# Optimization experiments

Hardware: AMD Instinct MI355X
Metric: run time of the kernel (lower is better)

## Reference

```python
import jax, jax.numpy as jnp
import numpy as np
from jax import lax

H, D_INNER, G, D_GATE, K, DH = 2560, 8192, 32, 4096, 4, 128
EPS = 1e-6


def setup_inputs() -> dict:
    key = jax.random.key(0)
    ks = jax.random.split(key, 9)
    B, L = 2, 4096
    s = 0.02
    return {
        "hidden_states": jax.random.normal(ks[0], (B, L, H), jnp.float32),
        "W_qkv": jax.random.normal(ks[1], (D_INNER, H), jnp.float32) * s,
        "W_b": jax.random.normal(ks[2], (G, H), jnp.float32) * s,
        "W_a": jax.random.normal(ks[3], (G, H), jnp.float32) * s,
        "conv_w": jax.random.normal(ks[4], (D_INNER, 1, K), jnp.float32) * s,
        "W_out": jax.random.normal(ks[5], (H, D_GATE), jnp.float32) * s,
        "norm_w": jnp.ones((DH,), jnp.float32),
        "A_log": jax.random.normal(ks[6], (G,), jnp.float32) * 0.1,
        "dt_bias": jax.random.normal(ks[7], (G,), jnp.float32) * 0.1,
    }


def _ssm_scan(x, B_coeff, C_coeff, A_log, dt_bias):
    # x: [B,L,G,DH], B_coeff/C_coeff: [B,L,G]
    A = -jnp.exp(A_log.astype(jnp.float32))          # [G]
    dt = jax.nn.softplus(dt_bias.astype(jnp.float32))  # [G]
    dA = jnp.exp(dt * A)                              # [G], time-invariant decay
    xf = x.astype(jnp.float32).transpose(1, 0, 2, 3)      # [L,B,G,DH]
    Bf = B_coeff.astype(jnp.float32).transpose(1, 0, 2)   # [L,B,G]
    Cf = C_coeff.astype(jnp.float32).transpose(1, 0, 2)
    h0 = jnp.zeros(x.shape[0:1] + (G, DH), jnp.float32)   # [B,G,DH]

    def step(h, inp):
        x_t, b_t, c_t = inp
        h = dA[None, :, None] * h + (dt * b_t)[..., None] * x_t
        return h, c_t[..., None] * h

    _, ys = lax.scan(step, h0, (xf, Bf, Cf))  # ys: [L,B,G,DH]
    return ys.transpose(1, 0, 2, 3).astype(x.dtype)


def reference(hidden_states, W_qkv, W_b, W_a, conv_w, W_out, norm_w, A_log, dt_bias):
    Bsz, L, _ = hidden_states.shape
    xz = hidden_states @ W_qkv.T           # [B,L,8192]
    B_coeff = hidden_states @ W_b.T        # [B,L,32]
    C_coeff = hidden_states @ W_a.T        # [B,L,32]
    # causal depthwise conv1d (padding K-1 on left, right pad trimmed)
    xz_c = lax.conv_general_dilated(
        xz.transpose(0, 2, 1), conv_w, (1,), [(K - 1, 0)],
        feature_group_count=D_INNER,
        dimension_numbers=("NCH", "OIH", "NCH"))
    xz_c = xz_c.transpose(0, 2, 1)          # [B,L,8192]
    x, z_inner = jnp.split(xz_c, 2, axis=-1)  # each [B,L,4096]
    x = jax.nn.silu(x).reshape(Bsz, L, G, DH)
    y = _ssm_scan(x, B_coeff, C_coeff, A_log, dt_bias)  # [B,L,G,DH]
    # RMSNorm over head_dim
    y = y * lax.rsqrt(jnp.mean(y * y, axis=-1, keepdims=True) + EPS) * norm_w
    y = y.reshape(Bsz, L, D_GATE) * jax.nn.silu(z_inner)
    return y @ W_out.T                      # [B,L,2560]
```

## Files before the change

### kernel.cpp

```cpp
#include <hip/hip_runtime.h>
#include <cstdint>
#include <cstddef>

#define H_DIM   2560
#define DINNER  8192
#define GHEADS  32
#define DGATE   4096
#define DH      128
#define BSZ     2
#define LSEQ    4096
#define MROWS   (BSZ*LSEQ)
#define NXPAD   4352
#define NCHUNK  64
#define SCHUNK  (LSEQ/NCHUNK)

typedef __attribute__((ext_vector_type(4))) float    f32x4;
typedef __attribute__((ext_vector_type(8))) _Float16 f16x8;
typedef unsigned short u16;
typedef unsigned int   u32;

static __device__ __forceinline__ u16 f2h(float f) {
  _Float16 h = (_Float16)f;
  union { _Float16 h; u16 u; } v; v.h = h; return v.u;
}
static __device__ __forceinline__ float h2f(u16 u) {
  union { u16 u; _Float16 h; } v; v.u = u; return (float)v.h;
}
static __device__ __forceinline__ float silu(float x) {
  return x / (1.0f + expf(-x));
}

__global__ void cast_f32_f16(const float* __restrict__ in, u16* __restrict__ out, int n4) {
  int i = blockIdx.x * blockDim.x + threadIdx.x;
  if (i < n4) {
    f32x4 v = ((const f32x4*)in)[i];
    u32 p0 = (u32)f2h(v[0]) | ((u32)f2h(v[1]) << 16);
    u32 p1 = (u32)f2h(v[2]) | ((u32)f2h(v[3]) << 16);
    ((uint2*)out)[i] = make_uint2(p0, p1);
  }
}

__global__ void build_wc(const float* __restrict__ Wqkv, const float* __restrict__ Wb,
                         const float* __restrict__ Wa, u16* __restrict__ wcp,
                         u16* __restrict__ wz) {
  int row = blockIdx.x;
  if (row >= NXPAD) {
    const float* src = Wqkv + (size_t)(4096 + row - NXPAD) * H_DIM;
    u16* oh = wz + (size_t)(row - NXPAD) * H_DIM;
    for (int i = threadIdx.x; i < H_DIM / 4; i += blockDim.x) {
      f32x4 v = ((const f32x4*)src)[i];
      ((uint2*)oh)[i] = make_uint2((u32)f2h(v[0]) | ((u32)f2h(v[1]) << 16),
                                   (u32)f2h(v[2]) | ((u32)f2h(v[3]) << 16));
    }
    return;
  }
  const float* src = nullptr;
  if (row < 4096)              src = Wqkv + (size_t)row * H_DIM;
  else if (row < 4128)         src = Wb + (size_t)(row - 4096) * H_DIM;
  else if (row < 4160)         src = Wa + (size_t)(row - 4128) * H_DIM;
  u16* oh = wcp + (size_t)row * H_DIM;
  for (int i = threadIdx.x; i < H_DIM / 4; i += blockDim.x) {
    u32 p0 = 0, p1 = 0;
    if (src) {
      f32x4 v = ((const f32x4*)src)[i];
      p0 = (u32)f2h(v[0]) | ((u32)f2h(v[1]) << 16);
      p1 = (u32)f2h(v[2]) | ((u32)f2h(v[3]) << 16);
    }
    ((uint2*)oh)[i] = make_uint2(p0, p1);
  }
}

static __device__ __forceinline__ void gload16(const u16* g, u16* l) {
  __builtin_amdgcn_global_load_lds(
      (const __attribute__((address_space(1))) u32*)g,
      (__attribute__((address_space(3))) u32*)l, 16, 0, 0);
}

template<bool OUT_F16>
__global__ __launch_bounds__(512)
void gemm_h(const u16* __restrict__ A, const u16* __restrict__ Bt,
            void* __restrict__ Cout, int K, int ldc, int nbx, int cpx) {
  __shared__ __align__(16) u16 As0[128 * 32];
  __shared__ __align__(16) u16 As1[128 * 32];
  __shared__ __align__(16) u16 Bs0[256 * 32];
  __shared__ __align__(16) u16 Bs1[256 * 32];
  const int tid  = threadIdx.x;
  const int lane = tid & 63;
  const int wave = tid >> 6;
  const int wm = (wave & 1) * 64;
  const int wn = (wave >> 1) * 64;
  const int bid = blockIdx.x;
  const int lsw = (bid & 7) * cpx + (bid >> 3);
  const int by  = lsw / nbx;
  const int bx  = lsw - by * nbx;
  const size_t bm = (size_t)by * 128;
  const size_t bn = (size_t)bx * 256;

  const int eA = tid * 8;
  const int rA = eA >> 5, cA = eA & 31;
  const int rB0 = rA, cB0 = cA;
  const int rB1 = 128 + rA;

  const u16* Ab = A + bm * (size_t)K;
  const u16* Bb = Bt + bn * (size_t)K;

  f32x4 acc[4][4];
#pragma unroll
  for (int i = 0; i < 4; i++)
#pragma unroll
    for (int j = 0; j < 4; j++) acc[i][j] = (f32x4){0.f, 0.f, 0.f, 0.f};

#define STAGE(AS, BS, kk)                                              \
  do {                                                                 \
    gload16(Ab + (size_t)rA * K + (kk) + cA, &AS[wave * 512]);         \
    gload16(Bb + (size_t)rB0 * K + (kk) + cB0, &BS[wave * 512]);       \
    gload16(Bb + (size_t)rB1 * K + (kk) + cB0, &BS[4096 + wave * 512]);\
  } while (0)

#define COMPUTE(AS, BS)                                                          \
  do {                                                                           \
    const int fr = lane & 15, fk = (lane >> 4) * 8;                              \
    f16x8 av[4], bv[4];                                                          \
    _Pragma("unroll")                                                            \
    for (int i = 0; i < 4; i++) av[i] = *(const f16x8*)&AS[(wm + i * 16 + fr) * 32 + fk]; \
    _Pragma("unroll")                                                            \
    for (int j = 0; j < 4; j++) bv[j] = *(const f16x8*)&BS[(wn + j * 16 + fr) * 32 + fk]; \
    _Pragma("unroll")                                                            \
    for (int i = 0; i < 4; i++)                                                  \
      _Pragma("unroll")                                                          \
      for (int j = 0; j < 4; j++)                                                \
        acc[i][j] = __builtin_amdgcn_mfma_f32_16x16x32_f16(av[i], bv[j], acc[i][j], 0, 0, 0); \
  } while (0)

  STAGE(As0, Bs0, 0);
  __syncthreads();
  for (int k0 = 0; k0 < K; k0 += 64) {
    if (k0 + 32 < K) STAGE(As1, Bs1, k0 + 32);
    COMPUTE(As0, Bs0);
    __syncthreads();
    if (k0 + 64 < K) STAGE(As0, Bs0, k0 + 64);
    COMPUTE(As1, Bs1);
    __syncthreads();
  }
#undef STAGE
#undef COMPUTE

  const int cr = (lane >> 4) * 4, ccol = lane & 15;
#pragma unroll
  for (int i = 0; i < 4; i++)
#pragma unroll
    for (int j = 0; j < 4; j++)
#pragma unroll
      for (int r = 0; r < 4; r++) {
        size_t row = bm + wm + i * 16 + cr + r;
        size_t col = bn + wn + j * 16 + ccol;
        if (OUT_F16) ((u16*)Cout)[row * ldc + col] = f2h(acc[i][j][r]);
        else         ((float*)Cout)[row * ldc + col] = acc[i][j][r];
      }
}

__global__ __launch_bounds__(64)
void scan_pass1(const float* __restrict__ xzx, const float* __restrict__ conv_w,
                const float* __restrict__ A_log, const float* __restrict__ dt_bias,
                float* __restrict__ E) {
  const int bid = blockIdx.x;
  const int c   = bid & (NCHUNK - 1);
  const int bg  = bid >> 6;
  const int g   = bg & (GHEADS - 1);
  const int b   = bg >> 5;
  const int lane = threadIdx.x;
  const int ch0 = g * DH + lane, ch1 = ch0 + 64;

  const f32x4 w0 = ((const f32x4*)conv_w)[ch0];
  const f32x4 w1 = ((const f32x4*)conv_w)[ch1];
  const float dt = log1pf(expf(dt_bias[g]));
  const float Ac = -expf(A_log[g]);
  const float dA = expf(dt * Ac);

  const int l0 = c * SCHUNK;
  const float* base = xzx + (size_t)b * LSEQ * NXPAD;

  float xm3 = 0, xm2 = 0, xm1 = 0, Xm3 = 0, Xm2 = 0, Xm1 = 0;
#pragma unroll
  for (int j = 0; j < 3; j++) {
    int l = l0 - 3 + j;
    float v0 = 0, v1 = 0;
    if (l >= 0) {
      const float* rp = base + (size_t)l * NXPAD;
      v0 = rp[ch0]; v1 = rp[ch1];
    }
    if (j == 0) { xm3 = v0; Xm3 = v1; }
    else if (j == 1) { xm2 = v0; Xm2 = v1; }
    else { xm1 = v0; Xm1 = v1; }
  }
  float h0 = 0.f, h1 = 0.f;
  for (int t = 0; t < SCHUNK; t++) {
    const float* rp = base + (size_t)(l0 + t) * NXPAD;
    float xc0 = rp[ch0], xc1 = rp[ch1];
    float cx0 = w0[0] * xm3 + w0[1] * xm2 + w0[2] * xm1 + w0[3] * xc0;
    float cx1 = w1[0] * Xm3 + w1[1] * Xm2 + w1[2] * Xm1 + w1[3] * xc1;
    xm3 = xm2; xm2 = xm1; xm1 = xc0;
    Xm3 = Xm2; Xm2 = Xm1; Xm1 = xc1;
    float u = dt * rp[DGATE + g];
    h0 = dA * h0 + u * silu(cx0);
    h1 = dA * h1 + u * silu(cx1);
  }
  float* ep = E + (size_t)bid * DH;
  ep[lane] = h0; ep[lane + 64] = h1;
}

__global__ __launch_bounds__(64)
void scan_pass2(const float* __restrict__ E, float* __restrict__ Hs,
                const float* __restrict__ A_log, const float* __restrict__ dt_bias) {
  const int bg = blockIdx.x;
  const int g = bg & (GHEADS - 1);
  const int lane = threadIdx.x;
  const float dt = log1pf(expf(dt_bias[g]));
  const float Ac = -expf(A_log[g]);
  const float dAS = expf(dt * Ac * (float)SCHUNK);
  float h0 = 0.f, h1 = 0.f;
  for (int c = 0; c < NCHUNK; c++) {
    size_t idx = ((size_t)bg * NCHUNK + c) * DH;
    Hs[idx + lane] = h0; Hs[idx + lane + 64] = h1;
    h0 = dAS * h0 + E[idx + lane];
    h1 = dAS * h1 + E[idx + lane + 64];
  }
}

__global__ __launch_bounds__(64)
void scan_pass3(const float* __restrict__ xzx, const u16* __restrict__ xzz,
                const float* __restrict__ conv_w,
                const float* __restrict__ A_log, const float* __restrict__ dt_bias,
                const float* __restrict__ norm_w, const float* __restrict__ Hs,
                u16* __restrict__ gbuf) {
  const int bid = blockIdx.x;
  const int c   = bid & (NCHUNK - 1);
  const int bg  = bid >> 6;
  const int g   = bg & (GHEADS - 1);
  const int b   = bg >> 5;
  const int lane = threadIdx.x;
  const int ch0 = g * DH + lane, ch1 = ch0 + 64;

  const f32x4 wx0 = ((const f32x4*)conv_w)[ch0];
  const f32x4 wx1 = ((const f32x4*)conv_w)[ch1];
  const f32x4 wz0 = ((const f32x4*)conv_w)[DGATE + ch0];
  const f32x4 wz1 = ((const f32x4*)conv_w)[DGATE + ch1];
  const float nw0 = norm_w[lane], nw1 = norm_w[lane + 64];

  const float dt = log1pf(expf(dt_bias[g]));
  const float Ac = -expf(A_log[g]);
  const float dA = expf(dt * Ac);

  const int l0 = c * SCHUNK;
  const float* basex = xzx + (size_t)b * LSEQ * NXPAD;
  const u16*   basez = xzz + (size_t)b * LSEQ * DGATE;

  float xm3 = 0, xm2 = 0, xm1 = 0, Xm3 = 0, Xm2 = 0, Xm1 = 0;
  float zm3 = 0, zm2 = 0, zm1 = 0, Zm3 = 0, Zm2 = 0, Zm1 = 0;
#pragma unroll
  for (int j = 0; j < 3; j++) {
    int l = l0 - 3 + j;
    float vx0 = 0, vx1 = 0, vz0 = 0, vz1 = 0;
    if (l >= 0) {
      const float* rp = basex + (size_t)l * NXPAD;
      const u16*   rz = basez + (size_t)l * DGATE;
      vx0 = rp[ch0]; vx1 = rp[ch1];
      vz0 = h2f(rz[ch0]); vz1 = h2f(rz[ch1]);
    }
    if (j == 0) { xm3 = vx0; Xm3 = vx1; zm3 = vz0; Zm3 = vz1; }
    else if (j == 1) { xm2 = vx0; Xm2 = vx1; zm2 = vz0; Zm2 = vz1; }
    else { xm1 = vx0; Xm1 = vx1; zm1 = vz0; Zm1 = vz1; }
  }
  float h0 = Hs[(size_t)bid * DH + lane];
  float h1 = Hs[(size_t)bid * DH + lane + 64];
  for (int t = 0; t < SCHUNK; t++) {
    const int l = l0 + t;
    const float* rp = basex + (size_t)l * NXPAD;
    const u16*   rz = basez + (size_t)l * DGATE;
    float xc0 = rp[ch0], xc1 = rp[ch1];
    float zc0 = h2f(rz[ch0]), zc1 = h2f(rz[ch1]);
    float cx0 = wx0[0] * xm3 + wx0[1] * xm2 + wx0[2] * xm1 + wx0[3] * xc0;
    float cx1 = wx1[0] * Xm3 + wx1[1] * Xm2 + wx1[2] * Xm1 + wx1[3] * xc1;
    float cz0 = wz0[0] * zm3 + wz0[1] * zm2 + wz0[2] * zm1 + wz0[3] * zc0;
    float cz1 = wz1[0] * Zm3 + wz1[1] * Zm2 + wz1[2] * Zm1 + wz1[3] * zc1;
    xm3 = xm2; xm2 = xm1; xm1 = xc0;  Xm3 = Xm2; Xm2 = Xm1; Xm1 = xc1;
    zm3 = zm2; zm2 = zm1; zm1 = zc0;  Zm3 = Zm2; Zm2 = Zm1; Zm1 = zc1;
    float bcl = rp[DGATE + g];
    float ccl = rp[DGATE + 32 + g];
    float u = dt * bcl;
    h0 = dA * h0 + u * silu(cx0);
    h1 = dA * h1 + u * silu(cx1);
    float y0 = ccl * h0, y1 = ccl * h1;
    float ss = y0 * y0 + y1 * y1;
    ss += __shfl_xor(ss, 32); ss += __shfl_xor(ss, 16); ss += __shfl_xor(ss, 8);
    ss += __shfl_xor(ss, 4);  ss += __shfl_xor(ss, 2);  ss += __shfl_xor(ss, 1);
    const float sc = rsqrtf(ss * (1.0f / DH) + 1e-6f);
    u16* op = gbuf + (size_t)(b * LSEQ + l) * DGATE + g * DH;
    op[lane]      = f2h(y0 * sc * nw0 * silu(cz0));
    op[lane + 64] = f2h(y1 * sc * nw1 * silu(cz1));
  }
}

extern "C" void kernel_launch(void* const* d_in, const int* in_sizes, int n_in,
                              void* d_out, int out_size, void* d_ws, size_t ws_size,
                              hipStream_t stream) {
  (void)in_sizes; (void)n_in; (void)out_size; (void)ws_size;
  const float* hs    = (const float*)d_in[0];
  const float* Wqkv  = (const float*)d_in[1];
  const float* Wb    = (const float*)d_in[2];
  const float* Wa    = (const float*)d_in[3];
  const float* convw = (const float*)d_in[4];
  const float* Wout  = (const float*)d_in[5];
  const float* normw = (const float*)d_in[6];
  const float* Alog  = (const float*)d_in[7];
  const float* dtb   = (const float*)d_in[8];
  float* out = (float*)d_out;

  char* ws = (char*)d_ws;
  size_t off = 0;
  auto alloc = [&](size_t bytes) { void* p = ws + off; off += (bytes + 255) & ~(size_t)255; return p; };
  float* xzx    = (float*)alloc((size_t)MROWS * NXPAD * 4);
  u16*   xzz    = (u16*)alloc((size_t)MROWS * DGATE * 2);
  u16*   wcp    = (u16*)alloc((size_t)NXPAD * H_DIM * 2);
  u16*   wz     = (u16*)alloc((size_t)DGATE * H_DIM * 2);
  (void)alloc((size_t)24 << 20);
  u16*   wout_h = (u16*)alloc((size_t)H_DIM * DGATE * 2);
  float* E      = (float*)alloc((size_t)BSZ * GHEADS * NCHUNK * DH * 4);
  float* Hst    = (float*)alloc((size_t)BSZ * GHEADS * NCHUNK * DH * 4);
  u16*   gbuf   = wcp;
  u16*   hs_h   = (u16*)d_out;

  const int n4_hs = MROWS * H_DIM / 4;
  cast_f32_f16<<<(n4_hs + 255) / 256, 256, 0, stream>>>(hs, hs_h, n4_hs);
  build_wc<<<NXPAD + DGATE, 256, 0, stream>>>(Wqkv, Wb, Wa, wcp, wz);
  const int n4_wo = H_DIM * DGATE / 4;
  cast_f32_f16<<<(n4_wo + 255) / 256, 256, 0, stream>>>(Wout, wout_h, n4_wo);

  gemm_h<false><<<1088, 512, 0, stream>>>(hs_h, wcp, xzx, H_DIM, NXPAD, 17, 136);
  gemm_h<true><<<1024, 512, 0, stream>>>(hs_h, wz, xzz, H_DIM, DGATE, 16, 128);

  scan_pass1<<<BSZ * GHEADS * NCHUNK, 64, 0, stream>>>(xzx, convw, Alog, dtb, E);
  scan_pass2<<<BSZ * GHEADS, 64, 0, stream>>>(E, Hst, Alog, dtb);
  scan_pass3<<<BSZ * GHEADS * NCHUNK, 64, 0, stream>>>(xzx, xzz, convw, Alog, dtb, normw, Hst, gbuf);

  gemm_h<false><<<640, 512, 0, stream>>>(gbuf, wout_h, out, DGATE, H_DIM, 10, 80);
}
```

Before: 860.4 us.

## Swizzle GEMM LDS layout and deepen async prefetch with partial vmcnt waits

Stores each 32-element k-slice in LDS with an XOR swizzle on the 8-element column groups, so the fragment reads avoid bank conflicts. Both LDS buffers are now prefetched ahead, and explicit s_waitcnt vmcnt(3) plus raw s_barrier replace __syncthreads, letting one stage's global-to-LDS loads stay in flight while the other buffer is consumed. It also raises wave priority around the MFMA block. The manual waitcnt/barrier scheme relies on exact counts of outstanding loads and adds extra barriers per iteration.

New measurement: 854.5 us. Within noise of the previous version (-0.7%).

```diff
diff --git a/kernel.cpp b/kernel.cpp
--- a/kernel.cpp
+++ b/kernel.cpp
@@ -75,6 +75,10 @@
       (const __attribute__((address_space(1))) u32*)g,
       (__attribute__((address_space(3))) u32*)l, 16, 0, 0);
 }
+
+#define BAR()    asm volatile("s_barrier" ::: "memory")
+#define WAITV3() asm volatile("s_waitcnt vmcnt(3)" ::: "memory")
+#define WAITV0() asm volatile("s_waitcnt vmcnt(0)" ::: "memory")
 
 template<bool OUT_F16>
 __global__ __launch_bounds__(512)
@@ -96,11 +100,8 @@
   const size_t bm = (size_t)by * 128;
   const size_t bn = (size_t)bx * 256;
 
-  const int eA = tid * 8;
-  const int rA = eA >> 5, cA = eA & 31;
-  const int rB0 = rA, cB0 = cA;
-  const int rB1 = 128 + rA;
-
+  const int srow = tid >> 2;
+  const int scol = (((tid & 3) ^ ((srow >> 1) & 3)) << 3);
   const u16* Ab = A + bm * (size_t)K;
   const u16* Bb = Bt + bn * (size_t)K;
 
@@ -110,37 +111,46 @@
 #pragma unroll
     for (int j = 0; j < 4; j++) acc[i][j] = (f32x4){0.f, 0.f, 0.f, 0.f};
 
-#define STAGE(AS, BS, kk)                                              \
-  do {                                                                 \
-    gload16(Ab + (size_t)rA * K + (kk) + cA, &AS[wave * 512]);         \
-    gload16(Bb + (size_t)rB0 * K + (kk) + cB0, &BS[wave * 512]);       \
-    gload16(Bb + (size_t)rB1 * K + (kk) + cB0, &BS[4096 + wave * 512]);\
+#define STAGE(AS, BS, kk)                                                \
+  do {                                                                   \
+    gload16(Ab + (size_t)srow * K + (kk) + scol, &AS[tid * 8]);          \
+    gload16(Bb + (size_t)srow * K + (kk) + scol, &BS[tid * 8]);          \
+    gload16(Bb + (size_t)(128 + srow) * K + (kk) + scol, &BS[4096 + tid * 8]); \
   } while (0)
 
-#define COMPUTE(AS, BS)                                                          \
-  do {                                                                           \
-    const int fr = lane & 15, fk = (lane >> 4) * 8;                              \
-    f16x8 av[4], bv[4];                                                          \
-    _Pragma("unroll")                                                            \
-    for (int i = 0; i < 4; i++) av[i] = *(const f16x8*)&AS[(wm + i * 16 + fr) * 32 + fk]; \
-    _Pragma("unroll")                                                            \
-    for (int j = 0; j < 4; j++) bv[j] = *(const f16x8*)&BS[(wn + j * 16 + fr) * 32 + fk]; \
-    _Pragma("unroll")                                                            \
-    for (int i = 0; i < 4; i++)                                                  \
-      _Pragma("unroll")                                                          \
-      for (int j = 0; j < 4; j++)                                                \
+#define COMPUTE(AS, BS)                                                           \
+  do {                                                                            \
+    const int fr = lane & 15;                                                     \
+    const int fo = (((lane >> 4) ^ ((fr >> 1) & 3)) << 3);    \
+    f16x8 av[4], bv[4];                                                           \
+    _Pragma("unroll")                                                             \
+    for (int i = 0; i < 4; i++) av[i] = *(const f16x8*)&AS[(wm + i * 16 + fr) * 32 + fo]; \
+    _Pragma("unroll")                                                             \
+    for (int j = 0; j < 4; j++) bv[j] = *(const f16x8*)&BS[(wn + j * 16 + fr) * 32 + fo]; \
+    __builtin_amdgcn_s_setprio(1);                                                \
+    _Pragma("unroll")                                                             \
+    for (int i = 0; i < 4; i++)                                                   \
+      _Pragma("unroll")                                                           \
+      for (int j = 0; j < 4; j++)                                                 \
         acc[i][j] = __builtin_amdgcn_mfma_f32_16x16x32_f16(av[i], bv[j], acc[i][j], 0, 0, 0); \
+    __builtin_amdgcn_s_setprio(0);                                                \
   } while (0)
 
   STAGE(As0, Bs0, 0);
-  __syncthreads();
+  STAGE(As1, Bs1, 32);
+  WAITV3();
+  BAR();
   for (int k0 = 0; k0 < K; k0 += 64) {
-    if (k0 + 32 < K) STAGE(As1, Bs1, k0 + 32);
     COMPUTE(As0, Bs0);
-    __syncthreads();
-    if (k0 + 64 < K) STAGE(As0, Bs0, k0 + 64);
+    BAR();
+    if (k0 + 64 < K) { STAGE(As0, Bs0, k0 + 64); WAITV3(); }
+    else             { WAITV0(); }
+    BAR();
     COMPUTE(As1, Bs1);
-    __syncthreads();
+    BAR();
+    if (k0 + 96 < K) { STAGE(As1, Bs1, k0 + 96); WAITV3(); }
+    else             { WAITV0(); }
+    BAR();
   }
 #undef STAGE
 #undef COMPUTE
```

## Replace GEMM with 256x256-tile kernel using swizzled LDS and interleaved pipeline

Applied to the files above, without the earlier changes.

The fp16 MFMA GEMM moves from 128x256 tiles with a 32-wide K step to 256x256 tiles with a 64-wide K step, so each wave holds 8x4 accumulator fragments. LDS rows are XOR-swizzled to avoid bank conflicts. The main loop interleaves async global-to-LDS loads, LDS reads and MFMA groups, using explicit s_barrier, vmcnt waits and s_setprio. The intent is more reuse per loaded byte and better overlap of memory and compute in all three GEMMs. The cost is fewer blocks (320–544), about 128KB of LDS per block, and higher register pressure.

New measurement: 854.1 us. About the same (-0.7%).

```diff
diff --git a/kernel.cpp b/kernel.cpp
--- a/kernel.cpp
+++ b/kernel.cpp
@@ -76,86 +76,127 @@
       (__attribute__((address_space(3))) u32*)l, 16, 0, 0);
 }
 
+#define BAR()    asm volatile("s_barrier" ::: "memory")
+#define WAITV4() asm volatile("s_waitcnt vmcnt(4)" ::: "memory")
+#define WAITV0() asm volatile("s_waitcnt vmcnt(0)" ::: "memory")
+
 template<bool OUT_F16>
-__global__ __launch_bounds__(512)
-void gemm_h(const u16* __restrict__ A, const u16* __restrict__ Bt,
-            void* __restrict__ Cout, int K, int ldc, int nbx, int cpx) {
-  __shared__ __align__(16) u16 As0[128 * 32];
-  __shared__ __align__(16) u16 As1[128 * 32];
-  __shared__ __align__(16) u16 Bs0[256 * 32];
-  __shared__ __align__(16) u16 Bs1[256 * 32];
+__global__ __launch_bounds__(512, 2)
+void gemm256(const u16* __restrict__ A, const u16* __restrict__ Bt,
+             void* __restrict__ Cout, int K, int ldc, int nbx, int cpx) {
+  __shared__ __align__(16) u16 As[2][256 * 64];
+  __shared__ __align__(16) u16 Bs[2][256 * 64];
   const int tid  = threadIdx.x;
   const int lane = tid & 63;
   const int wave = tid >> 6;
-  const int wm = (wave & 1) * 64;
-  const int wn = (wave >> 1) * 64;
-  const int bid = blockIdx.x;
-  const int lsw = (bid & 7) * cpx + (bid >> 3);
-  const int by  = lsw / nbx;
-  const int bx  = lsw - by * nbx;
-  const size_t bm = (size_t)by * 128;
-  const size_t bn = (size_t)bx * 256;
-
-  const int eA = tid * 8;
-  const int rA = eA >> 5, cA = eA & 31;
-  const int rB0 = rA, cB0 = cA;
-  const int rB1 = 128 + rA;
-
-  const u16* Ab = A + bm * (size_t)K;
-  const u16* Bb = Bt + bn * (size_t)K;
-
-  f32x4 acc[4][4];
-#pragma unroll
-  for (int i = 0; i < 4; i++)
+  const int wm   = wave & 1;
+  const int wn   = wave >> 1;
+  const int bid  = blockIdx.x;
+  const int lsw  = (bid & 7) * cpx + (bid >> 3);
+  const int by   = lsw / nbx;
+  const int bx   = lsw - by * nbx;
+  const u16* Ab = A  + (size_t)by * 256 * K;
+  const u16* Bb = Bt + (size_t)bx * 256 * K;
+
+  const int srow0 = tid >> 3;
+  const int scol  = (((tid & 7) ^ (srow0 & 7)) << 3);
+  const int fr  = lane & 15;
+  const int kg  = lane >> 4;
+  const int rsw = fr & 7;
+
+  f32x4 acc[8][4];
+#pragma unroll
+  for (int i = 0; i < 8; i++)
 #pragma unroll
     for (int j = 0; j < 4; j++) acc[i][j] = (f32x4){0.f, 0.f, 0.f, 0.f};
 
-#define STAGE(AS, BS, kk)                                              \
-  do {                                                                 \
-    gload16(Ab + (size_t)rA * K + (kk) + cA, &AS[wave * 512]);         \
-    gload16(Bb + (size_t)rB0 * K + (kk) + cB0, &BS[wave * 512]);       \
-    gload16(Bb + (size_t)rB1 * K + (kk) + cB0, &BS[4096 + wave * 512]);\
+  f16x8 av[4], bv[4];
+
+#define STAGEOP(dst, gb, kk)                                                     \
+  do {                                                                           \
+    _Pragma("unroll")                                                            \
+    for (int q = 0; q < 4; q++)                                                  \
+      gload16((gb) + (size_t)(srow0 + q * 64) * K + (kk) + scol,                 \
+              (dst) + (size_t)(q * 512 + tid) * 8);                              \
   } while (0)
 
-#define COMPUTE(AS, BS)                                                          \
+#define DSREAD_AV(d, qm, s)                                                      \
   do {                                                                           \
-    const int fr = lane & 15, fk = (lane >> 4) * 8;                              \
-    f16x8 av[4], bv[4];                                                          \
     _Pragma("unroll")                                                            \
-    for (int i = 0; i < 4; i++) av[i] = *(const f16x8*)&AS[(wm + i * 16 + fr) * 32 + fk]; \
+    for (int i = 0; i < 4; i++)                                                  \
+      av[i] = *(const f16x8*)&As[d][(wm * 128 + (qm) * 64 + i * 16 + fr) * 64 +  \
+                                    ((((s) * 4 + kg) ^ rsw) << 3)];              \
+  } while (0)
+
+#define DSREAD_BV(d, s)                                                          \
+  do {                                                                           \
     _Pragma("unroll")                                                            \
-    for (int j = 0; j < 4; j++) bv[j] = *(const f16x8*)&BS[(wn + j * 16 + fr) * 32 + fk]; \
+    for (int j = 0; j < 4; j++)                                                  \
+      bv[j] = *(const f16x8*)&Bs[d][(wn * 64 + j * 16 + fr) * 64 +               \
+                                    ((((s) * 4 + kg) ^ rsw) << 3)];              \
+  } while (0)
+
+#define MFMA16(qm)                                                               \
+  do {                                                                           \
+    __builtin_amdgcn_s_setprio(1);                                               \
     _Pragma("unroll")                                                            \
     for (int i = 0; i < 4; i++)                                                  \
       _Pragma("unroll")                                                          \
       for (int j = 0; j < 4; j++)                                                \
-        acc[i][j] = __builtin_amdgcn_mfma_f32_16x16x32_f16(av[i], bv[j], acc[i][j], 0, 0, 0); \
+        acc[(qm) * 4 + i][j] =                                                   \
+            __builtin_amdgcn_mfma_f32_16x16x32_f16(av[i], bv[j],                 \
+                                                   acc[(qm) * 4 + i][j], 0, 0, 0);\
+    __builtin_amdgcn_s_setprio(0);                                               \
   } while (0)
 
-  STAGE(As0, Bs0, 0);
-  __syncthreads();
-  for (int k0 = 0; k0 < K; k0 += 64) {
-    if (k0 + 32 < K) STAGE(As1, Bs1, k0 + 32);
-    COMPUTE(As0, Bs0);
-    __syncthreads();
-    if (k0 + 64 < K) STAGE(As0, Bs0, k0 + 64);
-    COMPUTE(As1, Bs1);
-    __syncthreads();
-  }
-#undef STAGE
-#undef COMPUTE
+  const int T = K >> 7;
+  STAGEOP(&Bs[0][0], Bb, 0);
+  STAGEOP(&As[0][0], Ab, 0);
+  STAGEOP(&Bs[1][0], Bb, 64);
+  WAITV4();
+  BAR();
+
+  for (int it = 0; it < T; ++it) {
+    const int k0 = it << 7;
+    const bool lastit = (it == T - 1);
+    DSREAD_BV(0, 0); DSREAD_AV(0, 0, 0);
+    STAGEOP(&As[1][0], Ab, k0 + 64);
+    BAR(); MFMA16(0); BAR();
+    DSREAD_AV(0, 1, 0);
+    BAR(); MFMA16(1); BAR();
+    DSREAD_BV(0, 1); DSREAD_AV(0, 0, 1);
+    BAR(); MFMA16(0); BAR();
+    DSREAD_AV(0, 1, 1);
+    if (!lastit) { STAGEOP(&Bs[0][0], Bb, k0 + 128); WAITV4(); }
+    else         { WAITV0(); }
+    BAR(); MFMA16(1); BAR();
+    DSREAD_BV(1, 0); DSREAD_AV(1, 0, 0);
+    if (!lastit) STAGEOP(&As[0][0], Ab, k0 + 128);
+    BAR(); MFMA16(0); BAR();
+    DSREAD_AV(1, 1, 0);
+    BAR(); MFMA16(1); BAR();
+    DSREAD_BV(1, 1); DSREAD_AV(1, 0, 1);
+    BAR(); MFMA16(0); BAR();
+    DSREAD_AV(1, 1, 1);
+    if (!lastit) { STAGEOP(&Bs[1][0], Bb, k0 + 192); WAITV4(); }
+    BAR(); MFMA16(1); BAR();
+  }
+#undef STAGEOP
+#undef DSREAD_AV
+#undef DSREAD_BV
+#undef MFMA16
 
   const int cr = (lane >> 4) * 4, ccol = lane & 15;
 #pragma unroll
-  for (int i = 0; i < 4; i++)
-#pragma unroll
-    for (int j = 0; j < 4; j++)
+  for (int mf = 0; mf < 8; mf++)
+#pragma unroll
+    for (int nf = 0; nf < 4; nf++)
 #pragma unroll
       for (int r = 0; r < 4; r++) {
-        size_t row = bm + wm + i * 16 + cr + r;
-        size_t col = bn + wn + j * 16 + ccol;
-        if (OUT_F16) ((u16*)Cout)[row * ldc + col] = f2h(acc[i][j][r]);
-        else         ((float*)Cout)[row * ldc + col] = acc[i][j][r];
+        size_t row = (size_t)by * 256 + wm * 128 + mf * 16 + cr + r;
+        size_t col = (size_t)bx * 256 + wn * 64 + nf * 16 + ccol;
+        if (OUT_F16) ((u16*)Cout)[row * ldc + col] = f2h(acc[mf][nf][r]);
+        else         ((float*)Cout)[row * ldc + col] = acc[mf][nf][r];
       }
 }
 
@@ -336,12 +377,12 @@
   const int n4_wo = H_DIM * DGATE / 4;
   cast_f32_f16<<<(n4_wo + 255) / 256, 256, 0, stream>>>(Wout, wout_h, n4_wo);
 
-  gemm_h<false><<<1088, 512, 0, stream>>>(hs_h, wcp, xzx, H_DIM, NXPAD, 17, 136);
-  gemm_h<true><<<1024, 512, 0, stream>>>(hs_h, wz, xzz, H_DIM, DGATE, 16, 128);
+  gemm256<false><<<544, 512, 0, stream>>>(hs_h, wcp, xzx, H_DIM, NXPAD, 17, 68);
+  gemm256<true><<<512, 512, 0, stream>>>(hs_h, wz, xzz, H_DIM, DGATE, 16, 64);
 
   scan_pass1<<<BSZ * GHEADS * NCHUNK, 64, 0, stream>>>(xzx, convw, Alog, dtb, E);
   scan_pass2<<<BSZ * GHEADS, 64, 0, stream>>>(E, Hst, Alog, dtb);
   scan_pass3<<<BSZ * GHEADS * NCHUNK, 64, 0, stream>>>(xzx, xzz, convw, Alog, dtb, normw, Hst, gbuf);
 
-  gemm_h<false><<<640, 512, 0, stream>>>(gbuf, wout_h, out, DGATE, H_DIM, 10, 80);
-}
+  gemm256<false><<<320, 512, 0, stream>>>(gbuf, wout_h, out, DGATE, H_DIM, 10, 40);
+}
```
